# Performance work log

Measured on AMD Instinct MI355X. Metric: run time of the kernel, lower is better.

The kernel has to match this reference:

```python
import jax, jax.numpy as jnp
import numpy as np

B, H, I = 131072, 128, 128  # batch, hidden_size, input_size (must be equal per source math)


def setup_inputs() -> dict:
    key = jax.random.key(0)
    ks = jax.random.split(key, 7)
    return {
        "x":   jax.random.normal(ks[0], (B, H), dtype=jnp.float32),
        "h_0": jax.random.normal(ks[1], (B, H), dtype=jnp.float32),
        "c_0": jax.random.normal(ks[2], (B, H), dtype=jnp.float32),
        "ih":  jax.random.normal(ks[3], (4 * H, I), dtype=jnp.float32) * 0.1,
        "hh":  jax.random.normal(ks[4], (4 * H, H), dtype=jnp.float32) * 0.1,
        "ib":  jax.random.normal(ks[5], (4 * H,), dtype=jnp.float32) * 0.1,
        "hb":  jax.random.normal(ks[6], (4 * H,), dtype=jnp.float32) * 0.1,
    }


def reference(x, h_0, c_0, ih, hh, ib, hb):
    hidden = hh.shape[1]
    # torch.split(ih, H) -> 4 chunks [H, I]; gate = x @ chunk (note: NOT chunk.T)
    ih4 = ih.reshape(4, hidden, -1)        # [4, H, I]
    hh4 = hh.reshape(4, hidden, hidden)    # [4, H, H]
    ib4 = ib.reshape(4, 1, hidden)
    hb4 = hb.reshape(4, 1, hidden)
    # combined gate GEMM: gates[g] = x @ ih4[g] + ib4[g] + h_0 @ hh4[g] + hb4[g]
    gates = (jnp.einsum('bh,ghi->gbi', x, ih4)
             + jnp.einsum('bh,ghk->gbk', h_0, hh4)
             + ib4 + hb4)                  # [4, B, H]
    I_g, F_g, G_g, O_g = gates[0], gates[1], gates[2], gates[3]
    c_1 = c_0 * jax.nn.sigmoid(F_g) + jax.nn.sigmoid(I_g) * jnp.tanh(G_g)
    h_1 = jax.nn.sigmoid(O_g) + jnp.tanh(c_1)  # faithful to source (additive, not gated)
    return (h_1, c_1, I_g, F_g, G_g, O_g)
```

## Files before the change

### kernel.cpp

```cpp
#include <hip/hip_runtime.h>
#include <hip/hip_bf16.h>

typedef __attribute__((ext_vector_type(8))) short short8;
typedef __attribute__((ext_vector_type(4))) float f32x4;

#define HSZ 128
#define BM  64
#define NT  512

__device__ __forceinline__ unsigned short f2bf(float f) {
    union { float f; unsigned int u; } c; c.f = f;
    return (unsigned short)((c.u + 0x7FFFu + ((c.u >> 16) & 1u)) >> 16);
}

__global__ void prep_kernel(const float* __restrict__ ih, const float* __restrict__ hh,
                            const float* __restrict__ ib, const float* __restrict__ hb,
                            unsigned short* __restrict__ Wp, float* __restrict__ bias) {
    int tid = blockIdx.x * blockDim.x + threadIdx.x;
    int col = tid >> 5;
    int kg  = tid & 31;
    int g = col >> 7, i = col & 127;
    short8 pk;
    #pragma unroll
    for (int j = 0; j < 8; ++j) {
        int k = kg * 8 + j;
        float v = (k < HSZ) ? ih[(g * HSZ + k) * HSZ + i]
                            : hh[(g * HSZ + (k - HSZ)) * HSZ + i];
        pk[j] = (short)f2bf(v);
    }
    *reinterpret_cast<short8*>(Wp + col * 256 + kg * 8) = pk;
    if (kg == 0) bias[col] = ib[col] + hb[col];
}

union SMem {
    unsigned short A[BM * 264];
    float T[8][2048];
};

__global__ __launch_bounds__(NT, 4)
void lstm_kernel(const float* __restrict__ x, const float* __restrict__ h0,
                 const float* __restrict__ c0,
                 const unsigned short* __restrict__ Wp,
                 const float* __restrict__ biasp,
                 float* __restrict__ out, long BH) {
    constexpr int PITCH = 264;
    __shared__ SMem sm;

    const int t = threadIdx.x;
    const long rowBase = (long)blockIdx.x * BM;

    {
        const float4* x4 = reinterpret_cast<const float4*>(x + rowBase * HSZ);
        const float4* h4 = reinterpret_cast<const float4*>(h0 + rowBase * HSZ);
        #pragma unroll
        for (int j = 0; j < 4; ++j) {
            int fi = t + j * NT;
            int row = fi >> 5;
            int c4  = fi & 31;
            float4 vx = x4[fi];
            float4 vh = h4[fi];
            ushort4 px; px.x = f2bf(vx.x); px.y = f2bf(vx.y); px.z = f2bf(vx.z); px.w = f2bf(vx.w);
            ushort4 ph; ph.x = f2bf(vh.x); ph.y = f2bf(vh.y); ph.z = f2bf(vh.z); ph.w = f2bf(vh.w);
            *reinterpret_cast<ushort4*>(&sm.A[row * PITCH + c4 * 4]) = px;
            *reinterpret_cast<ushort4*>(&sm.A[row * PITCH + HSZ + c4 * 4]) = ph;
        }
    }
    __syncthreads();

    const int lane = t & 63;
    const int wid  = t >> 6;
    const int wm = wid & 1;
    const int wn = wid >> 1;
    const int lr = lane & 15;
    const int lk = lane >> 4;

    const char* Ab = reinterpret_cast<const char*>(sm.A)
                   + (wm * 32 + lr) * (PITCH * 2) + lk * 16;
    const char* Wb = reinterpret_cast<const char*>(Wp)
                   + (wn * 32 + lr) * 512 + lk * 16;

    f32x4 acc[2][2][4] = {};

    #pragma unroll
    for (int ks = 0; ks < 8; ++ks) {
        short8 a0 = *reinterpret_cast<const short8*>(Ab + ks * 64);
        short8 a1 = *reinterpret_cast<const short8*>(Ab + 16 * (PITCH * 2) + ks * 64);
        #pragma unroll
        for (int g = 0; g < 4; ++g) {
            #pragma unroll
            for (int ni = 0; ni < 2; ++ni) {
                short8 w = *reinterpret_cast<const short8*>(
                    Wb + (g * 128 + ni * 16) * 512 + ks * 64);
                acc[0][ni][g] = __builtin_amdgcn_mfma_f32_16x16x32_bf16(w, a0, acc[0][ni][g], 0, 0, 0);
                acc[1][ni][g] = __builtin_amdgcn_mfma_f32_16x16x32_bf16(w, a1, acc[1][ni][g], 0, 0, 0);
            }
        }
    }

    f32x4 c0v[2][2];
    #pragma unroll
    for (int mi = 0; mi < 2; ++mi)
        #pragma unroll
        for (int ni = 0; ni < 2; ++ni) {
            long pos = (rowBase + wm * 32 + mi * 16 + lr) * HSZ
                     + wn * 32 + ni * 16 + lk * 4;
            c0v[mi][ni] = *reinterpret_cast<const f32x4*>(c0 + pos);
        }

    #pragma unroll
    for (int ni = 0; ni < 2; ++ni)
        #pragma unroll
        for (int g = 0; g < 4; ++g) {
            f32x4 bg = *reinterpret_cast<const f32x4*>(
                biasp + g * HSZ + wn * 32 + ni * 16 + lk * 4);
            acc[0][ni][g] += bg;
            acc[1][ni][g] += bg;
        }

    __syncthreads();

    float* wt = sm.T[wid];
    const long rbase = (rowBase + wm * 32) * (long)HSZ + wn * 32;
    const int rr0 = lane >> 3;
    const int gg0 = lane & 7;

    #pragma unroll
    for (int mi = 0; mi < 2; ++mi)
        #pragma unroll
        for (int ni = 0; ni < 2; ++ni) {
            int row = mi * 16 + lr;
            int g4  = ni * 4 + lk;
            f32x4 c1v, h1v;
            #pragma unroll
            for (int r = 0; r < 4; ++r) {
                float iv = acc[mi][ni][0][r];
                float fv = acc[mi][ni][1][r];
                float gv = acc[mi][ni][2][r];
                float ov = acc[mi][ni][3][r];
                float si = 1.f / (1.f + __expf(-iv));
                float sf = 1.f / (1.f + __expf(-fv));
                float tg = 1.f - 2.f / (__expf(2.f * gv) + 1.f);
                float so = 1.f / (1.f + __expf(-ov));
                float c1 = c0v[mi][ni][r] * sf + si * tg;
                float th = 1.f - 2.f / (__expf(2.f * c1) + 1.f);
                c1v[r] = c1;
                h1v[r] = so + th;
            }
            int idx = row * 32 + ((g4 ^ (row & 7)) * 4);
            *reinterpret_cast<f32x4*>(&wt[idx])        = c1v;
            *reinterpret_cast<f32x4*>(&wt[1024 + idx]) = h1v;
        }
    __builtin_amdgcn_wave_barrier();

    #pragma unroll
    for (int p = 0; p < 4; ++p) {
        int rr  = p * 8 + rr0;
        int idx = rr * 32 + ((gg0 ^ (rr & 7)) * 4);
        f32x4 vc = *reinterpret_cast<const f32x4*>(&wt[idx]);
        f32x4 vh = *reinterpret_cast<const f32x4*>(&wt[1024 + idx]);
        long rpos = rbase + (long)rr * HSZ + gg0 * 4;
        *reinterpret_cast<f32x4*>(out + BH + rpos) = vc;
        *reinterpret_cast<f32x4*>(out + rpos)      = vh;
    }
    __builtin_amdgcn_wave_barrier();

    #pragma unroll
    for (int g = 0; g < 4; ++g) {
        float* slot = wt + (g & 1) * 1024;
        #pragma unroll
        for (int mi = 0; mi < 2; ++mi)
            #pragma unroll
            for (int ni = 0; ni < 2; ++ni) {
                int row = mi * 16 + lr;
                int g4  = ni * 4 + lk;
                int idx = row * 32 + ((g4 ^ (row & 7)) * 4);
                *reinterpret_cast<f32x4*>(&slot[idx]) = acc[mi][ni][g];
            }
        __builtin_amdgcn_wave_barrier();
        #pragma unroll
        for (int p = 0; p < 4; ++p) {
            int rr  = p * 8 + rr0;
            int idx = rr * 32 + ((gg0 ^ (rr & 7)) * 4);
            f32x4 v = *reinterpret_cast<const f32x4*>(&slot[idx]);
            long rpos = rbase + (long)rr * HSZ + gg0 * 4;
            *reinterpret_cast<f32x4*>(out + (long)(2 + g) * BH + rpos) = v;
        }
        __builtin_amdgcn_wave_barrier();
    }
}

extern "C" void kernel_launch(void* const* d_in, const int* in_sizes, int n_in,
                              void* d_out, int out_size, void* d_ws, size_t ws_size,
                              hipStream_t stream) {
    const float* x  = (const float*)d_in[0];
    const float* h0 = (const float*)d_in[1];
    const float* c0 = (const float*)d_in[2];
    const float* ih = (const float*)d_in[3];
    const float* hh = (const float*)d_in[4];
    const float* ib = (const float*)d_in[5];
    const float* hb = (const float*)d_in[6];
    float* out = (float*)d_out;

    unsigned short* Wp = (unsigned short*)d_ws;
    float* bias = (float*)((char*)d_ws + 512 * 256 * 2);

    long BH = in_sizes[2];
    long B  = BH / HSZ;

    prep_kernel<<<64, 256, 0, stream>>>(ih, hh, ib, hb, Wp, bias);
    lstm_kernel<<<(int)(B / BM), NT, 0, stream>>>(x, h0, c0, Wp, bias, out, BH);
}
```

Measured before the change: 233.0 us.

## Repartition warp tiles to 16 rows by 64 columns per wave

Changes the per-wave tile from 32 rows x 32 hidden columns to 16 rows x 64 hidden columns across the 8 waves. Each wave now loads one A fragment per k-step but twice as many weight fragments from global memory/L2. The LDS transpose staging and its XOR swizzle are reworked to fit the wider 64-column tile. The wider tile yields full 256-byte contiguous output row segments, but it raises weight-read traffic per wave.

```diff
diff --git a/kernel.cpp b/kernel.cpp
--- a/kernel.cpp
+++ b/kernel.cpp
@@ -69,93 +69,84 @@
 
     const int lane = t & 63;
     const int wid  = t >> 6;
-    const int wm = wid & 1;
-    const int wn = wid >> 1;
+    const int wm = wid & 3;
+    const int wn = wid >> 2;
     const int lr = lane & 15;
     const int lk = lane >> 4;
 
     const char* Ab = reinterpret_cast<const char*>(sm.A)
-                   + (wm * 32 + lr) * (PITCH * 2) + lk * 16;
+                   + (wm * 16 + lr) * (PITCH * 2) + lk * 16;
     const char* Wb = reinterpret_cast<const char*>(Wp)
-                   + (wn * 32 + lr) * 512 + lk * 16;
-
-    f32x4 acc[2][2][4] = {};
+                   + (wn * 64 + lr) * 512 + lk * 16;
+
+    f32x4 acc[4][4] = {};
 
     #pragma unroll
     for (int ks = 0; ks < 8; ++ks) {
         short8 a0 = *reinterpret_cast<const short8*>(Ab + ks * 64);
-        short8 a1 = *reinterpret_cast<const short8*>(Ab + 16 * (PITCH * 2) + ks * 64);
         #pragma unroll
         for (int g = 0; g < 4; ++g) {
             #pragma unroll
-            for (int ni = 0; ni < 2; ++ni) {
+            for (int ni = 0; ni < 4; ++ni) {
                 short8 w = *reinterpret_cast<const short8*>(
                     Wb + (g * 128 + ni * 16) * 512 + ks * 64);
-                acc[0][ni][g] = __builtin_amdgcn_mfma_f32_16x16x32_bf16(w, a0, acc[0][ni][g], 0, 0, 0);
-                acc[1][ni][g] = __builtin_amdgcn_mfma_f32_16x16x32_bf16(w, a1, acc[1][ni][g], 0, 0, 0);
+                acc[ni][g] = __builtin_amdgcn_mfma_f32_16x16x32_bf16(w, a0, acc[ni][g], 0, 0, 0);
             }
         }
     }
 
-    f32x4 c0v[2][2];
-    #pragma unroll
-    for (int mi = 0; mi < 2; ++mi)
-        #pragma unroll
-        for (int ni = 0; ni < 2; ++ni) {
-            long pos = (rowBase + wm * 32 + mi * 16 + lr) * HSZ
-                     + wn * 32 + ni * 16 + lk * 4;
-            c0v[mi][ni] = *reinterpret_cast<const f32x4*>(c0 + pos);
-        }
-
-    #pragma unroll
-    for (int ni = 0; ni < 2; ++ni)
+    f32x4 c0v[4];
+    #pragma unroll
+    for (int ni = 0; ni < 4; ++ni) {
+        long pos = (rowBase + wm * 16 + lr) * HSZ + wn * 64 + ni * 16 + lk * 4;
+        c0v[ni] = *reinterpret_cast<const f32x4*>(c0 + pos);
+    }
+
+    #pragma unroll
+    for (int ni = 0; ni < 4; ++ni)
         #pragma unroll
         for (int g = 0; g < 4; ++g) {
             f32x4 bg = *reinterpret_cast<const f32x4*>(
-                biasp + g * HSZ + wn * 32 + ni * 16 + lk * 4);
-            acc[0][ni][g] += bg;
-            acc[1][ni][g] += bg;
+                biasp + g * HSZ + wn * 64 + ni * 16 + lk * 4);
+            acc[ni][g] += bg;
         }
 
     __syncthreads();
 
     float* wt = sm.T[wid];
-    const long rbase = (rowBase + wm * 32) * (long)HSZ + wn * 32;
-    const int rr0 = lane >> 3;
-    const int gg0 = lane & 7;
-
-    #pragma unroll
-    for (int mi = 0; mi < 2; ++mi)
-        #pragma unroll
-        for (int ni = 0; ni < 2; ++ni) {
-            int row = mi * 16 + lr;
-            int g4  = ni * 4 + lk;
-            f32x4 c1v, h1v;
-            #pragma unroll
-            for (int r = 0; r < 4; ++r) {
-                float iv = acc[mi][ni][0][r];
-                float fv = acc[mi][ni][1][r];
-                float gv = acc[mi][ni][2][r];
-                float ov = acc[mi][ni][3][r];
-                float si = 1.f / (1.f + __expf(-iv));
-                float sf = 1.f / (1.f + __expf(-fv));
-                float tg = 1.f - 2.f / (__expf(2.f * gv) + 1.f);
-                float so = 1.f / (1.f + __expf(-ov));
-                float c1 = c0v[mi][ni][r] * sf + si * tg;
-                float th = 1.f - 2.f / (__expf(2.f * c1) + 1.f);
-                c1v[r] = c1;
-                h1v[r] = so + th;
-            }
-            int idx = row * 32 + ((g4 ^ (row & 7)) * 4);
-            *reinterpret_cast<f32x4*>(&wt[idx])        = c1v;
-            *reinterpret_cast<f32x4*>(&wt[1024 + idx]) = h1v;
-        }
+    const long rbase = (rowBase + wm * 16) * (long)HSZ + wn * 64;
+    const int rr0 = lane >> 4;
+    const int gg0 = lane & 15;
+
+    #pragma unroll
+    for (int ni = 0; ni < 4; ++ni) {
+        int g4  = ni * 4 + lk;
+        int idx = lr * 64 + ((g4 ^ lr) & 15) * 4;
+        f32x4 c1v, h1v;
+        #pragma unroll
+        for (int r = 0; r < 4; ++r) {
+            float iv = acc[ni][0][r];
+            float fv = acc[ni][1][r];
+            float gv = acc[ni][2][r];
+            float ov = acc[ni][3][r];
+            float si = 1.f / (1.f + __expf(-iv));
+            float sf = 1.f / (1.f + __expf(-fv));
+            float tg = 1.f - 2.f / (__expf(2.f * gv) + 1.f);
+            float so = 1.f / (1.f + __expf(-ov));
+            float c1 = c0v[ni][r] * sf + si * tg;
+            float th = 1.f - 2.f / (__expf(2.f * c1) + 1.f);
+            c1v[r] = c1;
+            h1v[r] = so + th;
+        }
+        *reinterpret_cast<f32x4*>(&wt[idx])        = c1v;
+        *reinterpret_cast<f32x4*>(&wt[1024 + idx]) = h1v;
+    }
     __builtin_amdgcn_wave_barrier();
 
     #pragma unroll
     for (int p = 0; p < 4; ++p) {
-        int rr  = p * 8 + rr0;
-        int idx = rr * 32 + ((gg0 ^ (rr & 7)) * 4);
+        int rr  = p * 4 + rr0;
+        int idx = rr * 64 + ((gg0 ^ rr) & 15) * 4;
         f32x4 vc = *reinterpret_cast<const f32x4*>(&wt[idx]);
         f32x4 vh = *reinterpret_cast<const f32x4*>(&wt[1024 + idx]);
         long rpos = rbase + (long)rr * HSZ + gg0 * 4;
@@ -168,19 +159,16 @@
     for (int g = 0; g < 4; ++g) {
         float* slot = wt + (g & 1) * 1024;
         #pragma unroll
-        for (int mi = 0; mi < 2; ++mi)
-            #pragma unroll
-            for (int ni = 0; ni < 2; ++ni) {
-                int row = mi * 16 + lr;
-                int g4  = ni * 4 + lk;
-                int idx = row * 32 + ((g4 ^ (row & 7)) * 4);
-                *reinterpret_cast<f32x4*>(&slot[idx]) = acc[mi][ni][g];
-            }
+        for (int ni = 0; ni < 4; ++ni) {
+            int g4  = ni * 4 + lk;
+            int idx = lr * 64 + ((g4 ^ lr) & 15) * 4;
+            *reinterpret_cast<f32x4*>(&slot[idx]) = acc[ni][g];
+        }
         __builtin_amdgcn_wave_barrier();
         #pragma unroll
         for (int p = 0; p < 4; ++p) {
-            int rr  = p * 8 + rr0;
-            int idx = rr * 32 + ((gg0 ^ (rr & 7)) * 4);
+            int rr  = p * 4 + rr0;
+            int idx = rr * 64 + ((gg0 ^ rr) & 15) * 4;
             f32x4 v = *reinterpret_cast<const f32x4*>(&slot[idx]);
             long rpos = rbase + (long)rr * HSZ + gg0 * 4;
             *reinterpret_cast<f32x4*>(out + (long)(2 + g) * BH + rpos) = v;
```

Result: slower. 353.4 us (+51.7%).
